# Optimization experiments

Measured on AMD Instinct MI355X. Metric: run time of the kernel, lower is better.

Reference implementation:

```python
import math
import jax, jax.numpy as jnp
import numpy as np

EPS = 1e-12
NHEAD = 12
HEAD_DIM = 64  # d_model // nhead = 768 // 12


def setup_inputs() -> dict:
    key = jax.random.key(0)
    ks = jax.random.split(key, 8)
    L, D, H = 12, 768, 2048
    B, S = 8, 1024
    std = 0.02
    return {
        "x": jax.random.normal(ks[0], (B, S, D), jnp.float32),
        "wq": jax.random.normal(ks[1], (L, D, D), jnp.float32) * std,
        "wk": jax.random.normal(ks[2], (L, D, D), jnp.float32) * std,
        "wv": jax.random.normal(ks[3], (L, D, D), jnp.float32) * std,
        "wo": jax.random.normal(ks[4], (L, D, D), jnp.float32) * std,
        "w1": jax.random.normal(ks[5], (L, H, D), jnp.float32) * std,
        "w2": jax.random.normal(ks[6], (L, D, H), jnp.float32) * std,
        "attn_norm_w": jnp.ones((L, D), jnp.float32),
        "ffn_norm_w": jnp.ones((L, D), jnp.float32),
    }


def _rmsnorm(x, w):
    # x * rsqrt(mean(x^2) + eps) * w
    return x * jax.lax.rsqrt(jnp.mean(x * x, axis=-1, keepdims=True) + EPS) * w


def _block(x, params):
    wq, wk, wv, wo, w1, w2, anw, fnw = params
    B, S, D = x.shape
    # --- attention (manual matmul-softmax-matmul, fp32 softmax) ---
    xn = _rmsnorm(x, anw)
    q = jnp.einsum('bsd,ed->bse', xn, wq).reshape(B, S, NHEAD, HEAD_DIM)
    k = jnp.einsum('bsd,ed->bse', xn, wk).reshape(B, S, NHEAD, HEAD_DIM)
    v = jnp.einsum('bsd,ed->bse', xn, wv).reshape(B, S, NHEAD, HEAD_DIM)
    scores = jnp.einsum('bqhd,bkhd->bhqk', q, k) / math.sqrt(HEAD_DIM)
    probs = jax.nn.softmax(scores.astype(jnp.float32), axis=-1).astype(x.dtype)
    attn = jnp.einsum('bhqk,bkhd->bqhd', probs, v).reshape(B, S, D)
    h = x + jnp.einsum('bsd,ed->bse', attn, wo)
    # --- FFN: w2(silu(w1(h_norm))) ---
    hn = _rmsnorm(h, fnw)
    ff = jnp.einsum('bsh,dh->bsd', jax.nn.silu(jnp.einsum('bsd,hd->bsh', hn, w1)), w2)
    return h + ff


def reference(x, wq, wk, wv, wo, w1, w2, attn_norm_w, ffn_norm_w):
    def step(carry, p):
        return _block(carry, p), None
    out, _ = jax.lax.scan(step, x, (wq, wk, wv, wo, w1, w2, attn_norm_w, ffn_norm_w))
    return out
```

## Files before the change

### kernel.cpp

```cpp
#include <hip/hip_runtime.h>
#include <stdint.h>

typedef unsigned short u16;
typedef unsigned int u32;
typedef __bf16 bf16x8 __attribute__((ext_vector_type(8)));
typedef float f32x4 __attribute__((ext_vector_type(4)));

__device__ __forceinline__ u16 f2bf(float f) {
  u32 u = __builtin_bit_cast(u32, f);
  u32 r = (u + 0x7FFFu + ((u >> 16) & 1u)) >> 16;
  return (u16)r;
}

__global__ __launch_bounds__(256)
void convert_w(const float* __restrict__ wq, const float* __restrict__ wk,
               const float* __restrict__ wv, const float* __restrict__ wo,
               const float* __restrict__ w1, const float* __restrict__ w2,
               u16* __restrict__ out) {
  size_t i = ((size_t)blockIdx.x * 256 + threadIdx.x) * 4;
  if (i >= 5505024) return;
  const float* src; size_t off;
  if (i < 589824)       { src = wq; off = i; }
  else if (i < 1179648) { src = wk; off = i - 589824; }
  else if (i < 1769472) { src = wv; off = i - 1179648; }
  else if (i < 2359296) { src = wo; off = i - 1769472; }
  else if (i < 3932160) { src = w1; off = i - 2359296; }
  else                  { src = w2; off = i - 3932160; }
  float4 v = *(const float4*)(src + off);
  u32 lo = (u32)f2bf(v.x) | ((u32)f2bf(v.y) << 16);
  u32 hi = (u32)f2bf(v.z) | ((u32)f2bf(v.w) << 16);
  *(uint2*)(out + i) = make_uint2(lo, hi);
}

__device__ __forceinline__ void rn_store4(u16* p, float4 v, float4 w, float sc) {
  u32 lo = (u32)f2bf(v.x * sc * w.x) | ((u32)f2bf(v.y * sc * w.y) << 16);
  u32 hi = (u32)f2bf(v.z * sc * w.z) | ((u32)f2bf(v.w * sc * w.w) << 16);
  *(uint2*)p = make_uint2(lo, hi);
}

__global__ __launch_bounds__(256)
void rmsnorm_k(const float* __restrict__ x, const float* __restrict__ w,
               u16* __restrict__ out) {
  const int tok = (blockIdx.x << 2) + (threadIdx.x >> 6);
  const int l = threadIdx.x & 63;
  const float* xr = x + (size_t)tok * 768;
  float4 v0 = *(const float4*)(xr + l * 4);
  float4 v1 = *(const float4*)(xr + 256 + l * 4);
  float4 v2 = *(const float4*)(xr + 512 + l * 4);
  float ss = v0.x*v0.x + v0.y*v0.y + v0.z*v0.z + v0.w*v0.w
           + v1.x*v1.x + v1.y*v1.y + v1.z*v1.z + v1.w*v1.w
           + v2.x*v2.x + v2.y*v2.y + v2.z*v2.z + v2.w*v2.w;
  ss += __shfl_xor(ss, 1);  ss += __shfl_xor(ss, 2);  ss += __shfl_xor(ss, 4);
  ss += __shfl_xor(ss, 8);  ss += __shfl_xor(ss, 16); ss += __shfl_xor(ss, 32);
  float sc = rsqrtf(ss * (1.f / 768.f) + 1e-12f);
  float4 w0 = *(const float4*)(w + l * 4);
  float4 w1v = *(const float4*)(w + 256 + l * 4);
  float4 w2v = *(const float4*)(w + 512 + l * 4);
  u16* o = out + (size_t)tok * 768;
  rn_store4(o + l * 4, v0, w0, sc);
  rn_store4(o + 256 + l * 4, v1, w1v, sc);
  rn_store4(o + 512 + l * 4, v2, w2v, sc);
}

#define GEMM_CORE(A_, W_, K_, m0_, n0_)                                             \
  for (int kt = 0; kt < (K_); kt += 64) {                                           \
    __syncthreads();                                                                \
    _Pragma("unroll")                                                               \
    for (int ii = 0; ii < 4; ++ii) {                                                \
      int issue = (w << 2) + ii;                                                    \
      int r = (issue << 3) + (l >> 3);                                              \
      int c = (l & 7) ^ (r & 7);                                                    \
      __builtin_amdgcn_global_load_lds((A_) + (size_t)((m0_) + r) * (K_) + kt + c * 8, \
                                       As + issue * 512, 16, 0, 0);                 \
      __builtin_amdgcn_global_load_lds((W_) + (size_t)((n0_) + r) * (K_) + kt + c * 8, \
                                       Ws + issue * 512, 16, 0, 0);                 \
    }                                                                               \
    __syncthreads();                                                                \
    _Pragma("unroll")                                                               \
    for (int kc = 0; kc < 2; ++kc) {                                                \
      int chunk = lg + (kc << 2);                                                   \
      bf16x8 af[4], bfr[4];                                                         \
      _Pragma("unroll")                                                             \
      for (int i = 0; i < 4; ++i) {                                                 \
        int mr = (wm << 6) + (i << 4) + ll;                                         \
        af[i] = *(const bf16x8*)((const char*)As + mr * 128 + ((chunk ^ (mr & 7)) << 4)); \
        int nr = (wn << 6) + (i << 4) + ll;                                         \
        bfr[i] = *(const bf16x8*)((const char*)Ws + nr * 128 + ((chunk ^ (nr & 7)) << 4)); \
      }                                                                             \
      _Pragma("unroll")                                                             \
      for (int i = 0; i < 4; ++i)                                                   \
        _Pragma("unroll")                                                           \
        for (int j = 0; j < 4; ++j)                                                 \
          acc[i][j] = __builtin_amdgcn_mfma_f32_16x16x32_bf16(af[i], bfr[j], acc[i][j], 0, 0, 0); \
    }                                                                               \
  }

template<int EP>
__global__ __launch_bounds__(256, 2)
void gemm_bt(const u16* __restrict__ A, const u16* __restrict__ W,
             void* __restrict__ outp, const float* __restrict__ Res,
             int M, int N, int K) {
  __shared__ __align__(16) u16 As[128 * 64];
  __shared__ __align__(16) u16 Ws[128 * 64];
  const int tid = threadIdx.x;
  const int w = tid >> 6, l = tid & 63;
  const int lg = l >> 4, ll = l & 15;
  const int ntiles = N >> 7;
  const int mt = blockIdx.x / ntiles, nt = blockIdx.x - mt * ntiles;
  const int m0 = mt << 7, n0 = nt << 7;
  const int wm = w >> 1, wn = w & 1;

  const f32x4 fz = {0.f, 0.f, 0.f, 0.f};
  f32x4 acc[4][4];
#pragma unroll
  for (int i = 0; i < 4; ++i)
#pragma unroll
    for (int j = 0; j < 4; ++j) acc[i][j] = fz;

  GEMM_CORE(A, W, K, m0, n0)

  const int g4 = lg << 2;
#pragma unroll
  for (int i = 0; i < 4; ++i) {
#pragma unroll
    for (int j = 0; j < 4; ++j) {
      int row0 = m0 + (wm << 6) + (i << 4) + g4;
      int col = n0 + (wn << 6) + (j << 4) + ll;
      f32x4 v = acc[i][j];
      if (EP == 0) {
        u16* o = (u16*)outp;
#pragma unroll
        for (int e = 0; e < 4; ++e) o[(size_t)(row0 + e) * N + col] = f2bf(v[e]);
      } else if (EP == 1) {
        float* o = (float*)outp;
#pragma unroll
        for (int e = 0; e < 4; ++e) {
          size_t idx = (size_t)(row0 + e) * N + col;
          o[idx] = Res[idx] + v[e];
        }
      } else {
        u16* o = (u16*)outp;
#pragma unroll
        for (int e = 0; e < 4; ++e) {
          float xx = v[e];
          o[(size_t)(row0 + e) * N + col] = f2bf(xx / (1.f + __expf(-xx)));
        }
      }
    }
  }
}

__global__ __launch_bounds__(256, 2)
void gemm_qkv(const u16* __restrict__ A, const u16* __restrict__ W,
              u16* __restrict__ Qo, u16* __restrict__ Ko, u16* __restrict__ Vo) {
  __shared__ __align__(16) u16 As[128 * 64];
  __shared__ __align__(16) u16 Ws[128 * 64];
  const int tid = threadIdx.x;
  const int w = tid >> 6, l = tid & 63;
  const int lg = l >> 4, ll = l & 15;
  const int mt = blockIdx.x / 18, nt = blockIdx.x - mt * 18;
  const int m0 = mt << 7, n0 = nt << 7;
  const int wm = w >> 1, wn = w & 1;
  const int K = 768;

  const f32x4 fz = {0.f, 0.f, 0.f, 0.f};
  f32x4 acc[4][4];
#pragma unroll
  for (int i = 0; i < 4; ++i)
#pragma unroll
    for (int j = 0; j < 4; ++j) acc[i][j] = fz;

  GEMM_CORE(A, W, K, m0, n0)

  const int g4 = lg << 2;
#pragma unroll
  for (int i = 0; i < 4; ++i) {
#pragma unroll
    for (int j = 0; j < 4; ++j) {
      int row0 = m0 + (wm << 6) + (i << 4) + g4;
      int col = n0 + (wn << 6) + (j << 4) + ll;
      f32x4 v = acc[i][j];
      if (nt < 12) {
        u16* o = (nt < 6) ? Qo : Ko;
        int c = (nt < 6) ? col : (col - 768);
#pragma unroll
        for (int e = 0; e < 4; ++e) o[(size_t)(row0 + e) * 768 + c] = f2bf(v[e]);
      } else {
        int c = col - 1536;
        int vrow = ((row0 >> 10) * 768) + c;
        u32 lo = (u32)f2bf(v[0]) | ((u32)f2bf(v[1]) << 16);
        u32 hi = (u32)f2bf(v[2]) | ((u32)f2bf(v[3]) << 16);
        *(uint2*)(Vo + ((size_t)vrow << 10) + (row0 & 1023)) = make_uint2(lo, hi);
      }
    }
  }
}

__global__ __launch_bounds__(256, 2)
void attn_kernel(const u16* __restrict__ Q, const u16* __restrict__ Kg,
                 const u16* __restrict__ Vt, u16* __restrict__ Og) {
  __shared__ __align__(16) u16 Ks[128 * 64];
  __shared__ __align__(16) u16 Vs[64 * 128];
  __shared__ __align__(16) __bf16 Ps[4][32 * 128];
  __shared__ float red[4][32];

  const int tid = threadIdx.x;
  const int w = tid >> 6, l = tid & 63;
  const int lg = l >> 4, ll = l & 15;
  const int bid = blockIdx.x;
  const int qt = bid & 7, bh = bid >> 3;
  const int b = bh / 12, hh = bh - b * 12;

  bf16x8 qf[2][2];
  {
    const int tq = (b << 10) + (qt << 7) + (w << 5);
#pragma unroll
    for (int fm = 0; fm < 2; ++fm)
#pragma unroll
      for (int kc = 0; kc < 2; ++kc)
        qf[fm][kc] = *(const bf16x8*)(Q + (size_t)(tq + fm * 16 + ll) * 768 + hh * 64 + kc * 32 + lg * 8);
  }

  const f32x4 fz = {0.f, 0.f, 0.f, 0.f};
  f32x4 oacc[4][2];
#pragma unroll
  for (int i = 0; i < 4; ++i) { oacc[i][0] = fz; oacc[i][1] = fz; }
  float mrow[2][4], lrow[2][4];
#pragma unroll
  for (int fm = 0; fm < 2; ++fm)
#pragma unroll
    for (int j = 0; j < 4; ++j) { mrow[fm][j] = -1e30f; lrow[fm][j] = 0.f; }

  for (int kt = 0; kt < 8; ++kt) {
    __syncthreads();
#pragma unroll
    for (int ii = 0; ii < 4; ++ii) {
      int issue = (w << 2) + ii;
      int r = (issue << 3) + (l >> 3);
      int c = (l & 7) ^ (r & 7);
      __builtin_amdgcn_global_load_lds(
          Kg + (size_t)((b << 10) + (kt << 7) + r) * 768 + hh * 64 + c * 8,
          Ks + issue * 512, 16, 0, 0);
      int rv = (issue << 2) + (l >> 4);
      int cv = ll ^ (rv & 7);
      __builtin_amdgcn_global_load_lds(
          Vt + (size_t)((bh << 6) + rv) * 1024 + (kt << 7) + cv * 8,
          Vs + issue * 512, 16, 0, 0);
    }
    __syncthreads();

    f32x4 sa[2][8];
#pragma unroll
    for (int fm = 0; fm < 2; ++fm)
#pragma unroll
      for (int fn = 0; fn < 8; ++fn) sa[fm][fn] = fz;
#pragma unroll
    for (int kc = 0; kc < 2; ++kc) {
      int chunk = lg + (kc << 2);
      bf16x8 kb[8];
#pragma unroll
      for (int fn = 0; fn < 8; ++fn) {
        int nr = (fn << 4) + ll;
        kb[fn] = *(const bf16x8*)((const char*)Ks + nr * 128 + ((chunk ^ (nr & 7)) << 4));
      }
#pragma unroll
      for (int fm = 0; fm < 2; ++fm)
#pragma unroll
        for (int fn = 0; fn < 8; ++fn)
          sa[fm][fn] = __builtin_amdgcn_mfma_f32_16x16x32_bf16(qf[fm][kc], kb[fn], sa[fm][fn], 0, 0, 0);
    }
#pragma unroll
    for (int fm = 0; fm < 2; ++fm)
#pragma unroll
      for (int fn = 0; fn < 8; ++fn) sa[fm][fn] *= 0.125f;

#pragma unroll
    for (int fm = 0; fm < 2; ++fm) {
#pragma unroll
      for (int j = 0; j < 4; ++j) {
        float mx = sa[fm][0][j];
#pragma unroll
        for (int fn = 1; fn < 8; ++fn) mx = fmaxf(mx, sa[fm][fn][j]);
        mx = fmaxf(mx, __shfl_xor(mx, 1));
        mx = fmaxf(mx, __shfl_xor(mx, 2));
        mx = fmaxf(mx, __shfl_xor(mx, 4));
        mx = fmaxf(mx, __shfl_xor(mx, 8));
        float mold = mrow[fm][j];
        float mnew = fmaxf(mold, mx);
        float scal = __expf(mold - mnew);
        float rs = 0.f;
        int rq = (fm << 4) + (lg << 2) + j;
#pragma unroll
        for (int fn = 0; fn < 8; ++fn) {
          float p = __expf(sa[fm][fn][j] - mnew);
          rs += p;
          int kk = (fn << 4) + ll;
          Ps[w][rq * 128 + (((kk >> 3) ^ (rq & 7)) << 3) + (kk & 7)] =
              __builtin_bit_cast(__bf16, f2bf(p));
        }
        rs += __shfl_xor(rs, 1); rs += __shfl_xor(rs, 2);
        rs += __shfl_xor(rs, 4); rs += __shfl_xor(rs, 8);
        lrow[fm][j] = lrow[fm][j] * scal + rs;
        mrow[fm][j] = mnew;
        if (ll == 0) red[w][rq] = scal;
      }
    }

    asm volatile("" ::: "memory");

    float s0 = red[w][ll];
    float s1 = red[w][16 + ll];
#pragma unroll
    for (int i = 0; i < 4; ++i) { oacc[i][0] *= s0; oacc[i][1] *= s1; }

#pragma unroll
    for (int ch = 0; ch < 4; ++ch) {
      int chunk = lg + (ch << 2);
      bf16x8 pb[2];
#pragma unroll
      for (int fo = 0; fo < 2; ++fo) {
        int qr = (fo << 4) + ll;
        pb[fo] = *(const bf16x8*)((const char*)&Ps[w][0] + qr * 256 + ((chunk ^ (qr & 7)) << 4));
      }
#pragma unroll
      for (int fd = 0; fd < 4; ++fd) {
        int dr = (fd << 4) + ll;
        bf16x8 av = *(const bf16x8*)((const char*)Vs + dr * 256 + ((chunk ^ (dr & 7)) << 4));
        oacc[fd][0] = __builtin_amdgcn_mfma_f32_16x16x32_bf16(av, pb[0], oacc[fd][0], 0, 0, 0);
        oacc[fd][1] = __builtin_amdgcn_mfma_f32_16x16x32_bf16(av, pb[1], oacc[fd][1], 0, 0, 0);
      }
    }
  }

#pragma unroll
  for (int fm = 0; fm < 2; ++fm)
#pragma unroll
    for (int j = 0; j < 4; ++j)
      if (ll == 0) red[w][(fm << 4) + (lg << 2) + j] = lrow[fm][j];
  asm volatile("" ::: "memory");
  float inv0 = 1.f / red[w][ll];
  float inv1 = 1.f / red[w][16 + ll];
  const int tq0 = (b << 10) + (qt << 7) + (w << 5);
#pragma unroll
  for (int fd = 0; fd < 4; ++fd) {
#pragma unroll
    for (int fo = 0; fo < 2; ++fo) {
      int q = (fo << 4) + ll;
      float inv = fo ? inv1 : inv0;
      f32x4 v = oacc[fd][fo];
      int d0 = (fd << 4) + (lg << 2);
      u16* o = Og + (size_t)(tq0 + q) * 768 + hh * 64 + d0;
      u32 lo = (u32)f2bf(v[0] * inv) | ((u32)f2bf(v[1] * inv) << 16);
      u32 hi = (u32)f2bf(v[2] * inv) | ((u32)f2bf(v[3] * inv) << 16);
      *(uint2*)o = make_uint2(lo, hi);
    }
  }
}

extern "C" void kernel_launch(void* const* d_in, const int* in_sizes, int n_in,
                              void* d_out, int out_size, void* d_ws, size_t ws_size,
                              hipStream_t stream) {
  const float* x = (const float*)d_in[0];
  const float* wq = (const float*)d_in[1];
  const float* wk = (const float*)d_in[2];
  const float* wv = (const float*)d_in[3];
  const float* wo = (const float*)d_in[4];
  const float* w1 = (const float*)d_in[5];
  const float* w2 = (const float*)d_in[6];
  const float* anw = (const float*)d_in[7];
  const float* fnw = (const float*)d_in[8];

  char* ws = (char*)d_ws;
  float* h    = (float*)(ws);
  u16* xn     = (u16*)(ws + 25165824);
  u16* qb     = (u16*)(ws + 37748736);
  u16* kb     = (u16*)(ws + 50331648);
  u16* vt     = (u16*)(ws + 62914560);
  u16* ff1    = (u16*)(ws + 75497472);
  u16* wbuf   = (u16*)(ws + 109051904);

  hipMemcpyAsync(h, x, 25165824, hipMemcpyDeviceToDevice, stream);

  for (int L = 0; L < 12; ++L) {
    convert_w<<<5376, 256, 0, stream>>>(
        wq + (size_t)L * 589824, wk + (size_t)L * 589824,
        wv + (size_t)L * 589824, wo + (size_t)L * 589824,
        w1 + (size_t)L * 1572864, w2 + (size_t)L * 1572864, wbuf);
    rmsnorm_k<<<2048, 256, 0, stream>>>(h, anw + L * 768, xn);
    gemm_qkv<<<1152, 256, 0, stream>>>(xn, wbuf, qb, kb, vt);
    attn_kernel<<<768, 256, 0, stream>>>(qb, kb, vt, qb);
    gemm_bt<1><<<384, 256, 0, stream>>>(qb, wbuf + 1769472, h, h, 8192, 768, 768);
    rmsnorm_k<<<2048, 256, 0, stream>>>(h, fnw + L * 768, xn);
    gemm_bt<2><<<1024, 256, 0, stream>>>(xn, wbuf + 2359296, ff1, nullptr, 8192, 2048, 768);
    float* outw = (L == 11) ? (float*)d_out : h;
    gemm_bt<1><<<384, 256, 0, stream>>>(ff1, wbuf + 3932160, outw, h, 8192, 768, 2048);
  }
}
```

Baseline: 3.093 ms.

## Add 64-row GEMM tile for N=768 projections and slim attention P buffer

Adds a 64x128-tile GEMM with residual add, used for the output projection and the FFN down projection. It launches 768 blocks instead of 384 so the N=768 GEMMs fill more of the GPU. The attention kernel now runs its PV step per 16-row fragment, which halves the per-wave P shared-memory buffer and raises the occupancy hint to 3 blocks. It also folds log2(e) into the score scale so it can use exp2, and converts P to bf16 with a native cast. Smaller tiles reduce reuse per block, and the per-fragment PV loop adds extra serialization between softmax and MFMA.

```diff
diff --git a/kernel.cpp b/kernel.cpp
--- a/kernel.cpp
+++ b/kernel.cpp
@@ -150,6 +150,85 @@
   }
 }
 
+__global__ __launch_bounds__(256, 4)
+void gemm_bt64(const u16* __restrict__ A, const u16* __restrict__ W,
+               float* __restrict__ outp, const float* __restrict__ Res,
+               int M, int N, int K) {
+  __shared__ __align__(16) u16 As[64 * 64];
+  __shared__ __align__(16) u16 Ws[128 * 64];
+  const int tid = threadIdx.x;
+  const int w = tid >> 6, l = tid & 63;
+  const int lg = l >> 4, ll = l & 15;
+  const int ntiles = N >> 7;
+  const int mt = blockIdx.x / ntiles, nt = blockIdx.x - mt * ntiles;
+  const int m0 = mt << 6, n0 = nt << 7;
+  const int wm = w >> 1, wn = w & 1;
+
+  const f32x4 fz = {0.f, 0.f, 0.f, 0.f};
+  f32x4 acc[2][4];
+#pragma unroll
+  for (int i = 0; i < 2; ++i)
+#pragma unroll
+    for (int j = 0; j < 4; ++j) acc[i][j] = fz;
+
+  for (int kt = 0; kt < K; kt += 64) {
+    __syncthreads();
+#pragma unroll
+    for (int ii = 0; ii < 6; ++ii) {
+      int issue = w * 6 + ii;
+      if (issue < 8) {
+        int r = (issue << 3) + (l >> 3);
+        int c = (l & 7) ^ (r & 7);
+        __builtin_amdgcn_global_load_lds(A + (size_t)(m0 + r) * K + kt + c * 8,
+                                         As + issue * 512, 16, 0, 0);
+      } else {
+        int is2 = issue - 8;
+        int r = (is2 << 3) + (l >> 3);
+        int c = (l & 7) ^ (r & 7);
+        __builtin_amdgcn_global_load_lds(W + (size_t)(n0 + r) * K + kt + c * 8,
+                                         Ws + is2 * 512, 16, 0, 0);
+      }
+    }
+    __syncthreads();
+#pragma unroll
+    for (int kc = 0; kc < 2; ++kc) {
+      int chunk = lg + (kc << 2);
+      bf16x8 af[2], bfr[4];
+#pragma unroll
+      for (int i = 0; i < 2; ++i) {
+        int mr = (wm << 5) + (i << 4) + ll;
+        af[i] = *(const bf16x8*)((const char*)As + mr * 128 + ((chunk ^ (mr & 7)) << 4));
+      }
+#pragma unroll
+      for (int j = 0; j < 4; ++j) {
+        int nr = (wn << 6) + (j << 4) + ll;
+        bfr[j] = *(const bf16x8*)((const char*)Ws + nr * 128 + ((chunk ^ (nr & 7)) << 4));
+      }
+#pragma unroll
+      for (int i = 0; i < 2; ++i)
+#pragma unroll
+        for (int j = 0; j < 4; ++j)
+          acc[i][j] = __builtin_amdgcn_mfma_f32_16x16x32_bf16(af[i], bfr[j], acc[i][j], 0, 0, 0);
+    }
+  }
+
+  const int g4 = lg << 2;
+#pragma unroll
+  for (int i = 0; i < 2; ++i) {
+#pragma unroll
+    for (int j = 0; j < 4; ++j) {
+      int row0 = m0 + (wm << 5) + (i << 4) + g4;
+      int col = n0 + (wn << 6) + (j << 4) + ll;
+      f32x4 v = acc[i][j];
+#pragma unroll
+      for (int e = 0; e < 4; ++e) {
+        size_t idx = (size_t)(row0 + e) * N + col;
+        outp[idx] = Res[idx] + v[e];
+      }
+    }
+  }
+}
+
 __global__ __launch_bounds__(256, 2)
 void gemm_qkv(const u16* __restrict__ A, const u16* __restrict__ W,
               u16* __restrict__ Qo, u16* __restrict__ Ko, u16* __restrict__ Vo) {
@@ -196,12 +275,12 @@
   }
 }
 
-__global__ __launch_bounds__(256, 2)
+__global__ __launch_bounds__(256, 3)
 void attn_kernel(const u16* __restrict__ Q, const u16* __restrict__ Kg,
                  const u16* __restrict__ Vt, u16* __restrict__ Og) {
   __shared__ __align__(16) u16 Ks[128 * 64];
   __shared__ __align__(16) u16 Vs[64 * 128];
-  __shared__ __align__(16) __bf16 Ps[4][32 * 128];
+  __shared__ __align__(16) __bf16 Ps[4][16 * 128];
   __shared__ float red[4][32];
 
   const int tid = threadIdx.x;
@@ -210,6 +289,7 @@
   const int bid = blockIdx.x;
   const int qt = bid & 7, bh = bid >> 3;
   const int b = bh / 12, hh = bh - b * 12;
+  const float SC = 0.125f * 1.44269504f;
 
   bf16x8 qf[2][2];
   {
@@ -272,7 +352,7 @@
 #pragma unroll
     for (int fm = 0; fm < 2; ++fm)
 #pragma unroll
-      for (int fn = 0; fn < 8; ++fn) sa[fm][fn] *= 0.125f;
+      for (int fn = 0; fn < 8; ++fn) sa[fm][fn] *= SC;
 
 #pragma unroll
     for (int fm = 0; fm < 2; ++fm) {
@@ -287,16 +367,15 @@
         mx = fmaxf(mx, __shfl_xor(mx, 8));
         float mold = mrow[fm][j];
         float mnew = fmaxf(mold, mx);
-        float scal = __expf(mold - mnew);
+        float scal = __builtin_amdgcn_exp2f(mold - mnew);
         float rs = 0.f;
-        int rq = (fm << 4) + (lg << 2) + j;
+        int rq = (lg << 2) + j;
 #pragma unroll
         for (int fn = 0; fn < 8; ++fn) {
-          float p = __expf(sa[fm][fn][j] - mnew);
+          float p = __builtin_amdgcn_exp2f(sa[fm][fn][j] - mnew);
           rs += p;
           int kk = (fn << 4) + ll;
-          Ps[w][rq * 128 + (((kk >> 3) ^ (rq & 7)) << 3) + (kk & 7)] =
-              __builtin_bit_cast(__bf16, f2bf(p));
+          Ps[w][rq * 128 + (((kk >> 3) ^ (rq & 7)) << 3) + (kk & 7)] = (__bf16)p;
         }
         rs += __shfl_xor(rs, 1); rs += __shfl_xor(rs, 2);
         rs += __shfl_xor(rs, 4); rs += __shfl_xor(rs, 8);
@@ -304,31 +383,27 @@
         mrow[fm][j] = mnew;
         if (ll == 0) red[w][rq] = scal;
       }
-    }
-
-    asm volatile("" ::: "memory");
-
-    float s0 = red[w][ll];
-    float s1 = red[w][16 + ll];
-#pragma unroll
-    for (int i = 0; i < 4; ++i) { oacc[i][0] *= s0; oacc[i][1] *= s1; }
-
-#pragma unroll
-    for (int ch = 0; ch < 4; ++ch) {
-      int chunk = lg + (ch << 2);
-      bf16x8 pb[2];
-#pragma unroll
-      for (int fo = 0; fo < 2; ++fo) {
-        int qr = (fo << 4) + ll;
-        pb[fo] = *(const bf16x8*)((const char*)&Ps[w][0] + qr * 256 + ((chunk ^ (qr & 7)) << 4));
-      }
-#pragma unroll
-      for (int fd = 0; fd < 4; ++fd) {
-        int dr = (fd << 4) + ll;
-        bf16x8 av = *(const bf16x8*)((const char*)Vs + dr * 256 + ((chunk ^ (dr & 7)) << 4));
-        oacc[fd][0] = __builtin_amdgcn_mfma_f32_16x16x32_bf16(av, pb[0], oacc[fd][0], 0, 0, 0);
-        oacc[fd][1] = __builtin_amdgcn_mfma_f32_16x16x32_bf16(av, pb[1], oacc[fd][1], 0, 0, 0);
-      }
+
+      asm volatile("" ::: "memory");
+
+      float s0 = red[w][ll];
+#pragma unroll
+      for (int fd = 0; fd < 4; ++fd) oacc[fd][fm] *= s0;
+
+#pragma unroll
+      for (int ch = 0; ch < 4; ++ch) {
+        int chunk = lg + (ch << 2);
+        int qr = ll;
+        bf16x8 pb = *(const bf16x8*)((const char*)&Ps[w][0] + qr * 256 + ((chunk ^ (qr & 7)) << 4));
+#pragma unroll
+        for (int fd = 0; fd < 4; ++fd) {
+          int dr = (fd << 4) + ll;
+          bf16x8 av = *(const bf16x8*)((const char*)Vs + dr * 256 + ((chunk ^ (dr & 7)) << 4));
+          oacc[fd][fm] = __builtin_amdgcn_mfma_f32_16x16x32_bf16(av, pb, oacc[fd][fm], 0, 0, 0);
+        }
+      }
+
+      asm volatile("" ::: "memory");
     }
   }
 
@@ -389,10 +464,10 @@
     rmsnorm_k<<<2048, 256, 0, stream>>>(h, anw + L * 768, xn);
     gemm_qkv<<<1152, 256, 0, stream>>>(xn, wbuf, qb, kb, vt);
     attn_kernel<<<768, 256, 0, stream>>>(qb, kb, vt, qb);
-    gemm_bt<1><<<384, 256, 0, stream>>>(qb, wbuf + 1769472, h, h, 8192, 768, 768);
+    gemm_bt64<<<768, 256, 0, stream>>>(qb, wbuf + 1769472, h, h, 8192, 768, 768);
     rmsnorm_k<<<2048, 256, 0, stream>>>(h, fnw + L * 768, xn);
     gemm_bt<2><<<1024, 256, 0, stream>>>(xn, wbuf + 2359296, ff1, nullptr, 8192, 2048, 768);
     float* outw = (L == 11) ? (float*)d_out : h;
-    gemm_bt<1><<<384, 256, 0, stream>>>(ff1, wbuf + 3932160, outw, h, 8192, 768, 2048);
-  }
-}
+    gemm_bt64<<<768, 256, 0, stream>>>(ff1, wbuf + 3932160, outw, h, 8192, 768, 2048);
+  }
+}
```

Measured after the change: 3.907 ms. 1.26x slower.
